# Performance work log

Hardware: AMD Instinct MI355X
Metric: run time of the kernel (lower is better)

## Reference

```python
import jax, jax.numpy as jnp
import numpy as np

N, IN_DIM, MLPW, HID, NCLS = 2048, 1024, 16, 256, 4


def setup_inputs() -> dict:
    key = jax.random.key(0)
    ks = jax.random.split(key, 12)
    f32 = jnp.float32
    return {
        "x": jax.random.normal(ks[0], (N, IN_DIM), f32),
        "adj": jax.random.uniform(ks[1], (N, N), f32),
        "xdeg": jax.random.uniform(ks[2], (N, N), f32),
        "ydeg": jax.random.uniform(ks[3], (N, N), f32),
        # edge MLP([3, mlp_width, 2])
        "Wm1": jax.random.normal(ks[4], (3, MLPW), f32) * (1.0 / np.sqrt(3.0)),
        "bm1": jnp.zeros((MLPW,), f32),
        "Wm2": jax.random.normal(ks[5], (MLPW, 2), f32) * (1.0 / np.sqrt(MLPW)),
        "bm2": jnp.zeros((2,), f32),
        # GCN / dense layers (stored as [in, out]; torch Linear applies x @ W.T)
        "Wg1": jax.random.normal(ks[6], (IN_DIM, HID), f32) * (1.0 / np.sqrt(IN_DIM)),
        "Wl2": jax.random.normal(ks[7], (HID, 64), f32) * (1.0 / np.sqrt(HID)),
        "bl2": jnp.zeros((64,), f32),
        "Wg2": jax.random.normal(ks[8], (64, NCLS), f32) * (1.0 / 8.0),
    }


def reference(x, adj, xdeg, ydeg, Wm1, bm1, Wm2, bm2, Wg1, Wl2, bl2, Wg2):
    n = adj.shape[0]
    # Edge-feature MLP mask. The torch code gathers nonzero entries, runs the
    # MLP, scatters back into a zero buffer, then multiplies by adj. Computing
    # the mask densely is mathematically identical because adj * mask is zero
    # wherever adj is zero.
    feats = jnp.stack([adj, xdeg, ydeg], axis=-1)          # [N, N, 3]
    h = jax.nn.relu(feats @ Wm1 + bm1)                     # [N, N, MLPW]
    mask = jax.nn.softmax(h @ Wm2 + bm2, axis=-1)[..., 1]  # [N, N]
    A = adj * mask + jnp.eye(n, dtype=adj.dtype)
    # Symmetric-ish normalization: D_row^{-1/2} A D_col^{-1/2}
    # (the torch diag-matmul chain reduces to this row/col scaling).
    rowsum = jnp.sum(A, axis=1)
    colsum = jnp.sum(A, axis=0)
    dr = jnp.where(rowsum > 0, jax.lax.rsqrt(jnp.where(rowsum > 0, rowsum, 1.0)), 0.0)
    dc = jnp.where(colsum > 0, jax.lax.rsqrt(jnp.where(colsum > 0, colsum, 1.0)), 0.0)
    A = dr[:, None] * A * dc[None, :]
    # GCN layer 1 (dropout = identity in eval mode)
    hid = (A @ (x @ Wg1)) @ Wl2 + bl2                      # [N, 64]
    # GCN layer 2
    out = A @ (hid @ Wg2)                                  # [N, n_classes]
    return out, hid
```

## Files before the change

kernel.cpp:

```cpp
#include <hip/hip_runtime.h>

#define NN 2048
#define MLPW 16

typedef __attribute__((ext_vector_type(8))) short short8v;
typedef __attribute__((ext_vector_type(16))) float float16v;
typedef __attribute__((ext_vector_type(4))) unsigned short ushort4v;
typedef __attribute__((ext_vector_type(8))) unsigned short ushort8v;

__device__ __forceinline__ unsigned short f2b(float f) {
  unsigned int u = __float_as_uint(f);
  unsigned int r = (u + 0x7fffu + ((u >> 16) & 1u)) >> 16;
  return (unsigned short)r;
}
__device__ __forceinline__ float b2f(unsigned short u) {
  return __uint_as_float(((unsigned int)u) << 16);
}

__global__ void __launch_bounds__(256) edge_kernel(
    const float* __restrict__ adj, const float* __restrict__ xdeg,
    const float* __restrict__ ydeg,
    const float* __restrict__ Wm1, const float* __restrict__ bm1,
    const float* __restrict__ Wm2, const float* __restrict__ bm2,
    unsigned short* __restrict__ Abf, float* __restrict__ dr) {
  __shared__ float w1[48], b1[16], w2[32], b2s[2];
  __shared__ float wsum[4];
  const int tid = threadIdx.x;
  if (tid < 48) w1[tid] = Wm1[tid];
  if (tid < 16) b1[tid] = bm1[tid];
  if (tid < 32) w2[tid] = Wm2[tid];
  if (tid < 2) b2s[tid] = bm2[tid];
  __syncthreads();
  const int i = blockIdx.x;
  const float4* adj4 = (const float4*)(adj + (size_t)i * NN);
  const float4* xd4 = (const float4*)(xdeg + (size_t)i * NN);
  const float4* yd4 = (const float4*)(ydeg + (size_t)i * NN);
  ushort4v* A4 = (ushort4v*)(Abf + (size_t)i * NN);
  float rsum = 0.f;
  for (int j4 = tid; j4 < NN / 4; j4 += 256) {
    float4 av = adj4[j4], xv = xd4[j4], yv = yd4[j4];
    float aa[4] = {av.x, av.y, av.z, av.w};
    float xx[4] = {xv.x, xv.y, xv.z, xv.w};
    float yy[4] = {yv.x, yv.y, yv.z, yv.w};
    ushort4v oo;
#pragma unroll
    for (int e = 0; e < 4; e++) {
      float l0 = b2s[0], l1 = b2s[1];
#pragma unroll
      for (int k = 0; k < MLPW; k++) {
        float h = fmaf(aa[e], w1[k], fmaf(xx[e], w1[16 + k], fmaf(yy[e], w1[32 + k], b1[k])));
        h = fmaxf(h, 0.f);
        l0 = fmaf(h, w2[2 * k], l0);
        l1 = fmaf(h, w2[2 * k + 1], l1);
      }
      float mask = 1.f / (1.f + __expf(l0 - l1));
      float v = aa[e] * mask;
      int j = j4 * 4 + e;
      if (j == i) v += 1.f;
      oo[e] = f2b(v);
      rsum += v;
    }
    A4[j4] = oo;
  }
#pragma unroll
  for (int off = 32; off > 0; off >>= 1) rsum += __shfl_down(rsum, off);
  if ((tid & 63) == 0) wsum[tid >> 6] = rsum;
  __syncthreads();
  if (tid == 0) {
    float t = wsum[0] + wsum[1] + wsum[2] + wsum[3];
    dr[i] = t > 0.f ? rsqrtf(t) : 0.f;
  }
}

__global__ void __launch_bounds__(256) aux_kernel(
    const unsigned short* __restrict__ Abf, const float* __restrict__ x,
    const float* __restrict__ Wg1, float* __restrict__ partial,
    unsigned short* __restrict__ xb, unsigned short* __restrict__ Wg1T) {
  const int b = blockIdx.x, tid = threadIdx.x;
  if (b < 256) {
    const int j0 = tid * 8, i0 = b * 8;
    float s[8] = {0, 0, 0, 0, 0, 0, 0, 0};
#pragma unroll
    for (int i = 0; i < 8; i++) {
      ushort8v a = *(const ushort8v*)&Abf[(size_t)(i0 + i) * NN + j0];
#pragma unroll
      for (int e = 0; e < 8; e++) s[e] += b2f(a[e]);
    }
    float* p = partial + (size_t)b * NN + j0;
    *(float4*)p = make_float4(s[0], s[1], s[2], s[3]);
    *(float4*)(p + 4) = make_float4(s[4], s[5], s[6], s[7]);
  } else if (b < 1280) {
    const size_t idx = (size_t)(b - 256) * 2048 + (size_t)tid * 8;
    const float4 u = *(const float4*)&x[idx], v = *(const float4*)&x[idx + 4];
    ushort8v o = {f2b(u.x), f2b(u.y), f2b(u.z), f2b(u.w),
                  f2b(v.x), f2b(v.y), f2b(v.z), f2b(v.w)};
    *(ushort8v*)&xb[idx] = o;
  } else {
    const int bo = b - 1280;
    const int n = bo * 2 + (tid >> 7);
    const int k0 = (tid & 127) * 8;
    ushort8v o;
#pragma unroll
    for (int e = 0; e < 8; e++) o[e] = f2b(Wg1[(size_t)(k0 + e) * 256 + n]);
    *(ushort8v*)&Wg1T[(size_t)n * 1024 + k0] = o;
  }
}

__global__ void __launch_bounds__(256) dc_kernel(
    const float* __restrict__ partial, float* __restrict__ dc) {
  __shared__ float red[8][32];
  const int l = threadIdx.x & 31, g = threadIdx.x >> 5;
  const int col = blockIdx.x * 32 + l;
  float s = 0.f;
#pragma unroll
  for (int q = 0; q < 32; q++) s += partial[(size_t)(g * 32 + q) * NN + col];
  red[g][l] = s;
  __syncthreads();
  if (g == 0) {
    float t = s;
#pragma unroll
    for (int gg = 1; gg < 8; gg++) t += red[gg][l];
    dc[col] = t > 0.f ? rsqrtf(t) : 0.f;
  }
}

__global__ void __launch_bounds__(256) gemm_splitk_kernel(
    const unsigned short* __restrict__ A, const unsigned short* __restrict__ B,
    float* __restrict__ P, int M, int N, int K, int Kc) {
  constexpr int SW = 136;
  __shared__ unsigned short As[64 * SW];
  __shared__ unsigned short Bs[128 * SW];
  const int tid = threadIdx.x;
  const int lane = tid & 63, wave = tid >> 6;
  const int l31 = lane & 31, half = lane >> 5;
  const int mh = wave & 1, nh = wave >> 1;
  const int row0 = blockIdx.y * 64, col0 = blockIdx.x * 128;
  const int kbeg = blockIdx.z * Kc;

  float16v acc0, acc1;
#pragma unroll
  for (int r = 0; r < 16; r++) { acc0[r] = 0.f; acc1[r] = 0.f; }

  for (int k0 = 0; k0 < Kc; k0 += 128) {
#pragma unroll
    for (int i = 0; i < 4; i++) {
      const int id = tid + i * 256;
      const int r = id >> 4, c = id & 15;
      *(ushort8v*)&As[r * SW + c * 8] =
          *(const ushort8v*)&A[(size_t)(row0 + r) * K + kbeg + k0 + c * 8];
    }
#pragma unroll
    for (int i = 0; i < 8; i++) {
      const int id = tid + i * 256;
      const int r = id >> 4, c = id & 15;
      *(ushort8v*)&Bs[r * SW + c * 8] =
          *(const ushort8v*)&B[(size_t)(col0 + r) * K + kbeg + k0 + c * 8];
    }
    __syncthreads();
#pragma unroll
    for (int ks = 0; ks < 8; ks++) {
      short8v a = *(const short8v*)&As[(mh * 32 + l31) * SW + ks * 16 + half * 8];
      short8v b0 = *(const short8v*)&Bs[(nh * 64 + l31) * SW + ks * 16 + half * 8];
      short8v b1 = *(const short8v*)&Bs[(nh * 64 + 32 + l31) * SW + ks * 16 + half * 8];
      acc0 = __builtin_amdgcn_mfma_f32_32x32x16_bf16(a, b0, acc0, 0, 0, 0);
      acc1 = __builtin_amdgcn_mfma_f32_32x32x16_bf16(a, b1, acc1, 0, 0, 0);
    }
    __syncthreads();
  }
  float* Pb = P + ((size_t)blockIdx.z * M + row0 + mh * 32) * N + col0 + nh * 64 + l31;
#pragma unroll
  for (int reg = 0; reg < 16; reg++) {
    const int m = (reg & 3) + 8 * (reg >> 2) + 4 * half;
    Pb[(size_t)m * N] = acc0[reg];
    Pb[(size_t)m * N + 32] = acc1[reg];
  }
}

__global__ void __launch_bounds__(256) reduce_xwt_kernel(
    const float* __restrict__ P, const float* __restrict__ dc,
    unsigned short* __restrict__ XWT) {
  const int t = blockIdx.x * 256 + threadIdx.x;
  const int i = t >> 8;
  const int j0 = (t & 255) * 8;
  float s[8] = {0, 0, 0, 0, 0, 0, 0, 0};
#pragma unroll
  for (int sk = 0; sk < 8; sk++) {
    const float* p = P + ((size_t)sk * 256 + i) * 2048 + j0;
    float4 u = *(const float4*)p, v = *(const float4*)(p + 4);
    s[0] += u.x; s[1] += u.y; s[2] += u.z; s[3] += u.w;
    s[4] += v.x; s[5] += v.y; s[6] += v.z; s[7] += v.w;
  }
  float4 d0 = *(const float4*)&dc[j0], d1 = *(const float4*)&dc[j0 + 4];
  ushort8v o = {f2b(s[0] * d0.x), f2b(s[1] * d0.y), f2b(s[2] * d0.z), f2b(s[3] * d0.w),
                f2b(s[4] * d1.x), f2b(s[5] * d1.y), f2b(s[6] * d1.z), f2b(s[7] * d1.w)};
  *(ushort8v*)&XWT[(size_t)i * 2048 + j0] = o;
}

__global__ void __launch_bounds__(256) tail_kernel(
    const float* __restrict__ P2, const float* __restrict__ dr,
    const float* __restrict__ dc, const float* __restrict__ Wl2,
    const float* __restrict__ bl2, const float* __restrict__ Wg2,
    float* __restrict__ hid, float* __restrict__ HW) {
  __shared__ float T1s[8][256];
  __shared__ float hidS[8][68];
  const int m0 = blockIdx.x * 8;
  const int tid = threadIdx.x;
#pragma unroll
  for (int i = 0; i < 8; i++) {
    const int idx = tid + i * 256;
    const int mi = idx >> 8, n = idx & 255;
    float s = 0.f;
#pragma unroll
    for (int sk = 0; sk < 8; sk++)
      s += P2[((size_t)sk * 2048 + m0 + mi) * 256 + n];
    T1s[mi][n] = s * dr[m0 + mi];
  }
  __syncthreads();
  const int j = tid & 63, mg = tid >> 6;
  float h0 = bl2[j], h1 = h0;
  for (int n = 0; n < 256; n++) {
    float w = Wl2[(size_t)n * 64 + j];
    h0 = fmaf(T1s[mg * 2 + 0][n], w, h0);
    h1 = fmaf(T1s[mg * 2 + 1][n], w, h1);
  }
  hid[(size_t)(m0 + mg * 2 + 0) * 64 + j] = h0;
  hid[(size_t)(m0 + mg * 2 + 1) * 64 + j] = h1;
  hidS[mg * 2 + 0][j] = h0;
  hidS[mg * 2 + 1][j] = h1;
  __syncthreads();
  if (tid < 32) {
    const int r = tid >> 2, c = tid & 3;
    float s = 0.f;
#pragma unroll
    for (int jj = 0; jj < 64; jj++) s = fmaf(hidS[r][jj], Wg2[jj * 4 + c], s);
    HW[(size_t)(m0 + r) * 4 + c] = s * dc[m0 + r];
  }
}

__global__ void __launch_bounds__(256) out_kernel(
    const unsigned short* __restrict__ Abf, const float* __restrict__ HW,
    const float* __restrict__ dr, float* __restrict__ outp) {
  const int i = blockIdx.x, tid = threadIdx.x;
  const ushort8v a8 = ((const ushort8v*)(Abf + (size_t)i * NN))[tid];
  const float4* hw4 = (const float4*)HW;
  const int j0 = tid * 8;
  float ax = 0.f, ay = 0.f, az = 0.f, aw = 0.f;
#pragma unroll
  for (int e = 0; e < 8; e++) {
    float a = b2f(a8[e]);
    float4 h = hw4[j0 + e];
    ax = fmaf(a, h.x, ax);
    ay = fmaf(a, h.y, ay);
    az = fmaf(a, h.z, az);
    aw = fmaf(a, h.w, aw);
  }
#pragma unroll
  for (int off = 32; off > 0; off >>= 1) {
    ax += __shfl_down(ax, off);
    ay += __shfl_down(ay, off);
    az += __shfl_down(az, off);
    aw += __shfl_down(aw, off);
  }
  __shared__ float wsum[4][4];
  const int w = tid >> 6;
  if ((tid & 63) == 0) {
    wsum[w][0] = ax; wsum[w][1] = ay; wsum[w][2] = az; wsum[w][3] = aw;
  }
  __syncthreads();
  if (tid < 4)
    outp[(size_t)i * 4 + tid] =
        dr[i] * (wsum[0][tid] + wsum[1][tid] + wsum[2][tid] + wsum[3][tid]);
}

extern "C" void kernel_launch(void* const* d_in, const int* in_sizes, int n_in,
                              void* d_out, int out_size, void* d_ws, size_t ws_size,
                              hipStream_t stream) {
  const float* x    = (const float*)d_in[0];
  const float* adj  = (const float*)d_in[1];
  const float* xdeg = (const float*)d_in[2];
  const float* ydeg = (const float*)d_in[3];
  const float* Wm1  = (const float*)d_in[4];
  const float* bm1  = (const float*)d_in[5];
  const float* Wm2  = (const float*)d_in[6];
  const float* bm2  = (const float*)d_in[7];
  const float* Wg1  = (const float*)d_in[8];
  const float* Wl2  = (const float*)d_in[9];
  const float* bl2  = (const float*)d_in[10];
  const float* Wg2  = (const float*)d_in[11];

  char* ws = (char*)d_ws;
  unsigned short* Abf  = (unsigned short*)(ws);
  unsigned short* XWT  = (unsigned short*)(ws + 8388608);
  float* P     = (float*)(ws + 9437184);
  float* part  = (float*)(ws + 26214400);
  unsigned short* xb   = (unsigned short*)(ws + 28311552);
  unsigned short* Wg1T = (unsigned short*)(ws + 32505856);
  float* dr    = (float*)(ws + 33030144);
  float* dc    = (float*)(ws + 33038336);
  float* HW    = (float*)(ws + 33046528);

  float* outp = (float*)d_out;
  float* hid  = (float*)d_out + 2048 * 4;

  edge_kernel<<<NN, 256, 0, stream>>>(adj, xdeg, ydeg, Wm1, bm1, Wm2, bm2, Abf, dr);
  aux_kernel<<<1408, 256, 0, stream>>>(Abf, x, Wg1, part, xb, Wg1T);
  dc_kernel<<<64, 256, 0, stream>>>(part, dc);
  gemm_splitk_kernel<<<dim3(2048 / 128, 256 / 64, 8), 256, 0, stream>>>(
      Wg1T, xb, P, 256, 2048, 1024, 128);
  reduce_xwt_kernel<<<256, 256, 0, stream>>>(P, dc, XWT);
  gemm_splitk_kernel<<<dim3(256 / 128, 2048 / 64, 8), 256, 0, stream>>>(
      Abf, XWT, P, 2048, 256, 2048, 256);
  tail_kernel<<<2048 / 8, 256, 0, stream>>>(P, dr, dc, Wl2, bl2, Wg2, hid, HW);
  out_kernel<<<NN, 256, 0, stream>>>(Abf, HW, dr, outp);
}
```

Before: 172.6 us.

## Fuse edge MLP with fp32-staged X·Wg1 GEMM and merge dc/reduce kernels

```diff
diff --git a/kernel.cpp b/kernel.cpp
--- a/kernel.cpp
+++ b/kernel.cpp
@@ -17,111 +17,173 @@
   return __uint_as_float(((unsigned int)u) << 16);
 }
 
-__global__ void __launch_bounds__(256) edge_kernel(
+__global__ void __launch_bounds__(256, 4) fused1_kernel(
     const float* __restrict__ adj, const float* __restrict__ xdeg,
     const float* __restrict__ ydeg,
     const float* __restrict__ Wm1, const float* __restrict__ bm1,
     const float* __restrict__ Wm2, const float* __restrict__ bm2,
-    unsigned short* __restrict__ Abf, float* __restrict__ dr) {
-  __shared__ float w1[48], b1[16], w2[32], b2s[2];
-  __shared__ float wsum[4];
+    const float* __restrict__ x, const float* __restrict__ Wg1,
+    unsigned short* __restrict__ Abf, float* __restrict__ dr,
+    float* __restrict__ P1) {
+  constexpr int SW = 136;
+  __shared__ unsigned short As[64 * SW];
+  __shared__ unsigned short Bs[64 * SW];
+  __shared__ float w1[48], b1[16], w2[32], b2s[2], wsum[4];
   const int tid = threadIdx.x;
-  if (tid < 48) w1[tid] = Wm1[tid];
-  if (tid < 16) b1[tid] = bm1[tid];
-  if (tid < 32) w2[tid] = Wm2[tid];
-  if (tid < 2) b2s[tid] = bm2[tid];
-  __syncthreads();
-  const int i = blockIdx.x;
-  const float4* adj4 = (const float4*)(adj + (size_t)i * NN);
-  const float4* xd4 = (const float4*)(xdeg + (size_t)i * NN);
-  const float4* yd4 = (const float4*)(ydeg + (size_t)i * NN);
-  ushort4v* A4 = (ushort4v*)(Abf + (size_t)i * NN);
-  float rsum = 0.f;
-  for (int j4 = tid; j4 < NN / 4; j4 += 256) {
-    float4 av = adj4[j4], xv = xd4[j4], yv = yd4[j4];
-    float aa[4] = {av.x, av.y, av.z, av.w};
-    float xx[4] = {xv.x, xv.y, xv.z, xv.w};
-    float yy[4] = {yv.x, yv.y, yv.z, yv.w};
-    ushort4v oo;
-#pragma unroll
-    for (int e = 0; e < 4; e++) {
-      float l0 = b2s[0], l1 = b2s[1];
-#pragma unroll
-      for (int k = 0; k < MLPW; k++) {
-        float h = fmaf(aa[e], w1[k], fmaf(xx[e], w1[16 + k], fmaf(yy[e], w1[32 + k], b1[k])));
-        h = fmaxf(h, 0.f);
-        l0 = fmaf(h, w2[2 * k], l0);
-        l1 = fmaf(h, w2[2 * k + 1], l1);
+
+  if (blockIdx.x < 512) {
+    const int bg = blockIdx.x;
+    const int sk = bg >> 7, rem = bg & 127;
+    const int row0 = (rem >> 5) * 64;
+    const int col0 = (rem & 31) * 64;
+    const int kbeg = sk * 256;
+    const int lane = tid & 63, wave = tid >> 6;
+    const int l31 = lane & 31, half = lane >> 5;
+    const int mh2 = (wave & 1) * 32, nh2 = (wave >> 1) * 32;
+    const int k2 = (tid & 63) * 2;
+    const int mh = (tid >> 6) * 16;
+    const int rB = tid >> 2, cB = (tid & 3) * 32;
+
+    float16v acc;
+#pragma unroll
+    for (int r = 0; r < 16; r++) acc[r] = 0.f;
+
+    for (int k0 = 0; k0 < 256; k0 += 128) {
+      const float* a0 = Wg1 + (size_t)(kbeg + k0 + k2) * 256 + row0 + mh;
+      const float* a1 = a0 + 256;
+#pragma unroll
+      for (int q = 0; q < 4; q++) {
+        float4 va = ((const float4*)a0)[q];
+        float4 vb = ((const float4*)a1)[q];
+        ushort2 u;
+        u.x = f2b(va.x); u.y = f2b(vb.x); *(ushort2*)&As[(mh + q * 4 + 0) * SW + k2] = u;
+        u.x = f2b(va.y); u.y = f2b(vb.y); *(ushort2*)&As[(mh + q * 4 + 1) * SW + k2] = u;
+        u.x = f2b(va.z); u.y = f2b(vb.z); *(ushort2*)&As[(mh + q * 4 + 2) * SW + k2] = u;
+        u.x = f2b(va.w); u.y = f2b(vb.w); *(ushort2*)&As[(mh + q * 4 + 3) * SW + k2] = u;
       }
-      float mask = 1.f / (1.f + __expf(l0 - l1));
-      float v = aa[e] * mask;
-      int j = j4 * 4 + e;
-      if (j == i) v += 1.f;
-      oo[e] = f2b(v);
-      rsum += v;
-    }
-    A4[j4] = oo;
-  }
-#pragma unroll
-  for (int off = 32; off > 0; off >>= 1) rsum += __shfl_down(rsum, off);
-  if ((tid & 63) == 0) wsum[tid >> 6] = rsum;
-  __syncthreads();
-  if (tid == 0) {
-    float t = wsum[0] + wsum[1] + wsum[2] + wsum[3];
-    dr[i] = t > 0.f ? rsqrtf(t) : 0.f;
-  }
-}
-
-__global__ void __launch_bounds__(256) aux_kernel(
-    const unsigned short* __restrict__ Abf, const float* __restrict__ x,
-    const float* __restrict__ Wg1, float* __restrict__ partial,
-    unsigned short* __restrict__ xb, unsigned short* __restrict__ Wg1T) {
-  const int b = blockIdx.x, tid = threadIdx.x;
-  if (b < 256) {
-    const int j0 = tid * 8, i0 = b * 8;
-    float s[8] = {0, 0, 0, 0, 0, 0, 0, 0};
-#pragma unroll
-    for (int i = 0; i < 8; i++) {
-      ushort8v a = *(const ushort8v*)&Abf[(size_t)(i0 + i) * NN + j0];
-#pragma unroll
-      for (int e = 0; e < 8; e++) s[e] += b2f(a[e]);
-    }
-    float* p = partial + (size_t)b * NN + j0;
-    *(float4*)p = make_float4(s[0], s[1], s[2], s[3]);
-    *(float4*)(p + 4) = make_float4(s[4], s[5], s[6], s[7]);
-  } else if (b < 1280) {
-    const size_t idx = (size_t)(b - 256) * 2048 + (size_t)tid * 8;
-    const float4 u = *(const float4*)&x[idx], v = *(const float4*)&x[idx + 4];
-    ushort8v o = {f2b(u.x), f2b(u.y), f2b(u.z), f2b(u.w),
-                  f2b(v.x), f2b(v.y), f2b(v.z), f2b(v.w)};
-    *(ushort8v*)&xb[idx] = o;
+      const float* bp = x + (size_t)(col0 + rB) * 1024 + kbeg + k0 + cB;
+#pragma unroll
+      for (int q = 0; q < 4; q++) {
+        float4 u = ((const float4*)bp)[2 * q], v = ((const float4*)bp)[2 * q + 1];
+        ushort8v pk = {f2b(u.x), f2b(u.y), f2b(u.z), f2b(u.w),
+                       f2b(v.x), f2b(v.y), f2b(v.z), f2b(v.w)};
+        *(ushort8v*)&Bs[rB * SW + cB + q * 8] = pk;
+      }
+      __syncthreads();
+#pragma unroll
+      for (int ks = 0; ks < 8; ks++) {
+        short8v a = *(const short8v*)&As[(mh2 + l31) * SW + ks * 16 + half * 8];
+        short8v b = *(const short8v*)&Bs[(nh2 + l31) * SW + ks * 16 + half * 8];
+        acc = __builtin_amdgcn_mfma_f32_32x32x16_bf16(a, b, acc, 0, 0, 0);
+      }
+      __syncthreads();
+    }
+    float* Pb = P1 + ((size_t)sk * 256 + row0 + mh2) * NN + col0 + nh2 + l31;
+#pragma unroll
+    for (int reg = 0; reg < 16; reg++) {
+      const int m = (reg & 3) + 8 * (reg >> 2) + 4 * half;
+      Pb[(size_t)m * NN] = acc[reg];
+    }
   } else {
-    const int bo = b - 1280;
-    const int n = bo * 2 + (tid >> 7);
-    const int k0 = (tid & 127) * 8;
-    ushort8v o;
-#pragma unroll
-    for (int e = 0; e < 8; e++) o[e] = f2b(Wg1[(size_t)(k0 + e) * 256 + n]);
-    *(ushort8v*)&Wg1T[(size_t)n * 1024 + k0] = o;
-  }
-}
-
-__global__ void __launch_bounds__(256) dc_kernel(
-    const float* __restrict__ partial, float* __restrict__ dc) {
-  __shared__ float red[8][32];
-  const int l = threadIdx.x & 31, g = threadIdx.x >> 5;
-  const int col = blockIdx.x * 32 + l;
-  float s = 0.f;
-#pragma unroll
-  for (int q = 0; q < 32; q++) s += partial[(size_t)(g * 32 + q) * NN + col];
-  red[g][l] = s;
-  __syncthreads();
-  if (g == 0) {
-    float t = s;
-#pragma unroll
-    for (int gg = 1; gg < 8; gg++) t += red[gg][l];
-    dc[col] = t > 0.f ? rsqrtf(t) : 0.f;
-  }
+    if (tid < 48) w1[tid] = Wm1[tid];
+    if (tid < 16) b1[tid] = bm1[tid];
+    if (tid < 32) w2[tid] = Wm2[tid];
+    if (tid < 2) b2s[tid] = bm2[tid];
+    __syncthreads();
+    const int i = blockIdx.x - 512;
+    const float4* adj4 = (const float4*)(adj + (size_t)i * NN);
+    const float4* xd4 = (const float4*)(xdeg + (size_t)i * NN);
+    const float4* yd4 = (const float4*)(ydeg + (size_t)i * NN);
+    ushort4v* A4 = (ushort4v*)(Abf + (size_t)i * NN);
+    float rsum = 0.f;
+    for (int j4 = tid; j4 < NN / 4; j4 += 256) {
+      float4 av = adj4[j4], xv = xd4[j4], yv = yd4[j4];
+      float aa[4] = {av.x, av.y, av.z, av.w};
+      float xx[4] = {xv.x, xv.y, xv.z, xv.w};
+      float yy[4] = {yv.x, yv.y, yv.z, yv.w};
+      ushort4v oo;
+#pragma unroll
+      for (int e = 0; e < 4; e++) {
+        float l0 = b2s[0], l1 = b2s[1];
+#pragma unroll
+        for (int k = 0; k < MLPW; k++) {
+          float h = fmaf(aa[e], w1[k], fmaf(xx[e], w1[16 + k], fmaf(yy[e], w1[32 + k], b1[k])));
+          h = fmaxf(h, 0.f);
+          l0 = fmaf(h, w2[2 * k], l0);
+          l1 = fmaf(h, w2[2 * k + 1], l1);
+        }
+        float mask = 1.f / (1.f + __expf(l0 - l1));
+        float v = aa[e] * mask;
+        int j = j4 * 4 + e;
+        if (j == i) v += 1.f;
+        oo[e] = f2b(v);
+        rsum += v;
+      }
+      A4[j4] = oo;
+    }
+#pragma unroll
+    for (int off = 32; off > 0; off >>= 1) rsum += __shfl_down(rsum, off);
+    if ((tid & 63) == 0) wsum[tid >> 6] = rsum;
+    __syncthreads();
+    if (tid == 0) {
+      float t = wsum[0] + wsum[1] + wsum[2] + wsum[3];
+      dr[i] = t > 0.f ? rsqrtf(t) : 0.f;
+    }
+  }
+}
+
+__global__ void __launch_bounds__(256) dcxwt_kernel(
+    const unsigned short* __restrict__ Abf, const float* __restrict__ P1,
+    float* __restrict__ dc, unsigned short* __restrict__ XWT) {
+  __shared__ float partA[32][16];
+  __shared__ float dcs[16];
+  const int tid = threadIdx.x;
+  const int c0 = blockIdx.x * 16;
+  {
+    const int c2 = (tid & 7) * 2, rg = tid >> 3;
+    float s0 = 0.f, s1 = 0.f;
+    const unsigned short* ap = Abf + (size_t)rg * NN + c0 + c2;
+#pragma unroll 8
+    for (int k = 0; k < 64; k++) {
+      ushort2 u = *(const ushort2*)ap;
+      s0 += b2f(u.x);
+      s1 += b2f(u.y);
+      ap += 32 * NN;
+    }
+    partA[rg][c2] = s0;
+    partA[rg][c2 + 1] = s1;
+  }
+  __syncthreads();
+  if (tid < 16) {
+    float d = 0.f;
+#pragma unroll
+    for (int rg = 0; rg < 32; rg++) d += partA[rg][tid];
+    d = d > 0.f ? rsqrtf(d) : 0.f;
+    dcs[tid] = d;
+    dc[c0 + tid] = d;
+  }
+  __syncthreads();
+  float s[16];
+#pragma unroll
+  for (int e = 0; e < 16; e++) s[e] = 0.f;
+#pragma unroll
+  for (int sk = 0; sk < 4; sk++) {
+    const float* p = P1 + ((size_t)sk * 256 + tid) * NN + c0;
+    float4 u0 = ((const float4*)p)[0], u1 = ((const float4*)p)[1];
+    float4 u2 = ((const float4*)p)[2], u3 = ((const float4*)p)[3];
+    s[0] += u0.x; s[1] += u0.y; s[2] += u0.z; s[3] += u0.w;
+    s[4] += u1.x; s[5] += u1.y; s[6] += u1.z; s[7] += u1.w;
+    s[8] += u2.x; s[9] += u2.y; s[10] += u2.z; s[11] += u2.w;
+    s[12] += u3.x; s[13] += u3.y; s[14] += u3.z; s[15] += u3.w;
+  }
+  ushort8v o0 = {f2b(s[0] * dcs[0]), f2b(s[1] * dcs[1]), f2b(s[2] * dcs[2]),
+                 f2b(s[3] * dcs[3]), f2b(s[4] * dcs[4]), f2b(s[5] * dcs[5]),
+                 f2b(s[6] * dcs[6]), f2b(s[7] * dcs[7])};
+  ushort8v o1 = {f2b(s[8] * dcs[8]), f2b(s[9] * dcs[9]), f2b(s[10] * dcs[10]),
+                 f2b(s[11] * dcs[11]), f2b(s[12] * dcs[12]), f2b(s[13] * dcs[13]),
+                 f2b(s[14] * dcs[14]), f2b(s[15] * dcs[15])};
+  *(ushort8v*)&XWT[(size_t)tid * NN + c0] = o0;
+  *(ushort8v*)&XWT[(size_t)tid * NN + c0 + 8] = o1;
 }
 
 __global__ void __launch_bounds__(256) gemm_splitk_kernel(
@@ -176,35 +238,21 @@
   }
 }
 
-__global__ void __launch_bounds__(256) reduce_xwt_kernel(
-    const float* __restrict__ P, const float* __restrict__ dc,
-    unsigned short* __restrict__ XWT) {
-  const int t = blockIdx.x * 256 + threadIdx.x;
-  const int i = t >> 8;
-  const int j0 = (t & 255) * 8;
-  float s[8] = {0, 0, 0, 0, 0, 0, 0, 0};
-#pragma unroll
-  for (int sk = 0; sk < 8; sk++) {
-    const float* p = P + ((size_t)sk * 256 + i) * 2048 + j0;
-    float4 u = *(const float4*)p, v = *(const float4*)(p + 4);
-    s[0] += u.x; s[1] += u.y; s[2] += u.z; s[3] += u.w;
-    s[4] += v.x; s[5] += v.y; s[6] += v.z; s[7] += v.w;
-  }
-  float4 d0 = *(const float4*)&dc[j0], d1 = *(const float4*)&dc[j0 + 4];
-  ushort8v o = {f2b(s[0] * d0.x), f2b(s[1] * d0.y), f2b(s[2] * d0.z), f2b(s[3] * d0.w),
-                f2b(s[4] * d1.x), f2b(s[5] * d1.y), f2b(s[6] * d1.z), f2b(s[7] * d1.w)};
-  *(ushort8v*)&XWT[(size_t)i * 2048 + j0] = o;
-}
-
 __global__ void __launch_bounds__(256) tail_kernel(
     const float* __restrict__ P2, const float* __restrict__ dr,
     const float* __restrict__ dc, const float* __restrict__ Wl2,
     const float* __restrict__ bl2, const float* __restrict__ Wg2,
     float* __restrict__ hid, float* __restrict__ HW) {
   __shared__ float T1s[8][256];
+  __shared__ float Wl2s[256 * 64];
   __shared__ float hidS[8][68];
   const int m0 = blockIdx.x * 8;
   const int tid = threadIdx.x;
+#pragma unroll
+  for (int k = 0; k < 16; k++) {
+    const int idx = (tid + k * 256) * 4;
+    *(float4*)&Wl2s[idx] = *(const float4*)&Wl2[idx];
+  }
 #pragma unroll
   for (int i = 0; i < 8; i++) {
     const int idx = tid + i * 256;
@@ -218,8 +266,9 @@
   __syncthreads();
   const int j = tid & 63, mg = tid >> 6;
   float h0 = bl2[j], h1 = h0;
+#pragma unroll 8
   for (int n = 0; n < 256; n++) {
-    float w = Wl2[(size_t)n * 64 + j];
+    float w = Wl2s[n * 64 + j];
     h0 = fmaf(T1s[mg * 2 + 0][n], w, h0);
     h1 = fmaf(T1s[mg * 2 + 1][n], w, h1);
   }
@@ -289,27 +338,22 @@
   const float* Wg2  = (const float*)d_in[11];
 
   char* ws = (char*)d_ws;
-  unsigned short* Abf  = (unsigned short*)(ws);
-  unsigned short* XWT  = (unsigned short*)(ws + 8388608);
-  float* P     = (float*)(ws + 9437184);
-  float* part  = (float*)(ws + 26214400);
-  unsigned short* xb   = (unsigned short*)(ws + 28311552);
-  unsigned short* Wg1T = (unsigned short*)(ws + 32505856);
-  float* dr    = (float*)(ws + 33030144);
-  float* dc    = (float*)(ws + 33038336);
-  float* HW    = (float*)(ws + 33046528);
+  unsigned short* Abf = (unsigned short*)(ws);
+  float* P1   = (float*)(ws + 8388608);
+  unsigned short* XWT = (unsigned short*)(ws + 16777216);
+  float* P2   = (float*)(ws + 17825792);
+  float* dr   = (float*)(ws + 34603008);
+  float* dc   = (float*)(ws + 34611200);
+  float* HW   = (float*)(ws + 34619392);
 
   float* outp = (float*)d_out;
   float* hid  = (float*)d_out + 2048 * 4;
 
-  edge_kernel<<<NN, 256, 0, stream>>>(adj, xdeg, ydeg, Wm1, bm1, Wm2, bm2, Abf, dr);
-  aux_kernel<<<1408, 256, 0, stream>>>(Abf, x, Wg1, part, xb, Wg1T);
-  dc_kernel<<<64, 256, 0, stream>>>(part, dc);
-  gemm_splitk_kernel<<<dim3(2048 / 128, 256 / 64, 8), 256, 0, stream>>>(
-      Wg1T, xb, P, 256, 2048, 1024, 128);
-  reduce_xwt_kernel<<<256, 256, 0, stream>>>(P, dc, XWT);
+  fused1_kernel<<<2560, 256, 0, stream>>>(adj, xdeg, ydeg, Wm1, bm1, Wm2, bm2,
+                                          x, Wg1, Abf, dr, P1);
+  dcxwt_kernel<<<128, 256, 0, stream>>>(Abf, P1, dc, XWT);
   gemm_splitk_kernel<<<dim3(256 / 128, 2048 / 64, 8), 256, 0, stream>>>(
-      Abf, XWT, P, 2048, 256, 2048, 256);
-  tail_kernel<<<2048 / 8, 256, 0, stream>>>(P, dr, dc, Wl2, bl2, Wg2, hid, HW);
+      Abf, XWT, P2, 2048, 256, 2048, 256);
+  tail_kernel<<<2048 / 8, 256, 0, stream>>>(P2, dr, dc, Wl2, bl2, Wg2, hid, HW);
   out_kernel<<<NN, 256, 0, stream>>>(Abf, HW, dr, outp);
 }
```

Result: slower. 311.6 us (+80.6%).

## Fuse conversions into edge kernel and merge column-sum with split-K reduce

Applied to the files above, without the earlier changes.

```diff
diff --git a/kernel.cpp b/kernel.cpp
--- a/kernel.cpp
+++ b/kernel.cpp
@@ -22,16 +22,37 @@
     const float* __restrict__ ydeg,
     const float* __restrict__ Wm1, const float* __restrict__ bm1,
     const float* __restrict__ Wm2, const float* __restrict__ bm2,
-    unsigned short* __restrict__ Abf, float* __restrict__ dr) {
+    const float* __restrict__ x, const float* __restrict__ Wg1,
+    unsigned short* __restrict__ Abf, float* __restrict__ dr,
+    unsigned short* __restrict__ xb, unsigned short* __restrict__ Wg1T) {
+  const int tid = threadIdx.x;
+  const int b = blockIdx.x;
+  if (b >= 3072) {
+    const int bo = b - 3072;
+    const int n = bo * 2 + (tid >> 7);
+    const int k0 = (tid & 127) * 8;
+    ushort8v o;
+#pragma unroll
+    for (int e = 0; e < 8; e++) o[e] = f2b(Wg1[(size_t)(k0 + e) * 256 + n]);
+    *(ushort8v*)&Wg1T[(size_t)n * 1024 + k0] = o;
+    return;
+  }
+  if (b >= 2048) {
+    const size_t idx = (size_t)(b - 2048) * 2048 + (size_t)tid * 8;
+    const float4 u = *(const float4*)&x[idx], v = *(const float4*)&x[idx + 4];
+    ushort8v o = {f2b(u.x), f2b(u.y), f2b(u.z), f2b(u.w),
+                  f2b(v.x), f2b(v.y), f2b(v.z), f2b(v.w)};
+    *(ushort8v*)&xb[idx] = o;
+    return;
+  }
   __shared__ float w1[48], b1[16], w2[32], b2s[2];
   __shared__ float wsum[4];
-  const int tid = threadIdx.x;
   if (tid < 48) w1[tid] = Wm1[tid];
   if (tid < 16) b1[tid] = bm1[tid];
   if (tid < 32) w2[tid] = Wm2[tid];
   if (tid < 2) b2s[tid] = bm2[tid];
   __syncthreads();
-  const int i = blockIdx.x;
+  const int i = b;
   const float4* adj4 = (const float4*)(adj + (size_t)i * NN);
   const float4* xd4 = (const float4*)(xdeg + (size_t)i * NN);
   const float4* yd4 = (const float4*)(ydeg + (size_t)i * NN);
@@ -72,58 +93,6 @@
   }
 }
 
-__global__ void __launch_bounds__(256) aux_kernel(
-    const unsigned short* __restrict__ Abf, const float* __restrict__ x,
-    const float* __restrict__ Wg1, float* __restrict__ partial,
-    unsigned short* __restrict__ xb, unsigned short* __restrict__ Wg1T) {
-  const int b = blockIdx.x, tid = threadIdx.x;
-  if (b < 256) {
-    const int j0 = tid * 8, i0 = b * 8;
-    float s[8] = {0, 0, 0, 0, 0, 0, 0, 0};
-#pragma unroll
-    for (int i = 0; i < 8; i++) {
-      ushort8v a = *(const ushort8v*)&Abf[(size_t)(i0 + i) * NN + j0];
-#pragma unroll
-      for (int e = 0; e < 8; e++) s[e] += b2f(a[e]);
-    }
-    float* p = partial + (size_t)b * NN + j0;
-    *(float4*)p = make_float4(s[0], s[1], s[2], s[3]);
-    *(float4*)(p + 4) = make_float4(s[4], s[5], s[6], s[7]);
-  } else if (b < 1280) {
-    const size_t idx = (size_t)(b - 256) * 2048 + (size_t)tid * 8;
-    const float4 u = *(const float4*)&x[idx], v = *(const float4*)&x[idx + 4];
-    ushort8v o = {f2b(u.x), f2b(u.y), f2b(u.z), f2b(u.w),
-                  f2b(v.x), f2b(v.y), f2b(v.z), f2b(v.w)};
-    *(ushort8v*)&xb[idx] = o;
-  } else {
-    const int bo = b - 1280;
-    const int n = bo * 2 + (tid >> 7);
-    const int k0 = (tid & 127) * 8;
-    ushort8v o;
-#pragma unroll
-    for (int e = 0; e < 8; e++) o[e] = f2b(Wg1[(size_t)(k0 + e) * 256 + n]);
-    *(ushort8v*)&Wg1T[(size_t)n * 1024 + k0] = o;
-  }
-}
-
-__global__ void __launch_bounds__(256) dc_kernel(
-    const float* __restrict__ partial, float* __restrict__ dc) {
-  __shared__ float red[8][32];
-  const int l = threadIdx.x & 31, g = threadIdx.x >> 5;
-  const int col = blockIdx.x * 32 + l;
-  float s = 0.f;
-#pragma unroll
-  for (int q = 0; q < 32; q++) s += partial[(size_t)(g * 32 + q) * NN + col];
-  red[g][l] = s;
-  __syncthreads();
-  if (g == 0) {
-    float t = s;
-#pragma unroll
-    for (int gg = 1; gg < 8; gg++) t += red[gg][l];
-    dc[col] = t > 0.f ? rsqrtf(t) : 0.f;
-  }
-}
-
 __global__ void __launch_bounds__(256) gemm_splitk_kernel(
     const unsigned short* __restrict__ A, const unsigned short* __restrict__ B,
     float* __restrict__ P, int M, int N, int K, int Kc) {
@@ -176,24 +145,59 @@
   }
 }
 
-__global__ void __launch_bounds__(256) reduce_xwt_kernel(
-    const float* __restrict__ P, const float* __restrict__ dc,
-    unsigned short* __restrict__ XWT) {
-  const int t = blockIdx.x * 256 + threadIdx.x;
-  const int i = t >> 8;
-  const int j0 = (t & 255) * 8;
-  float s[8] = {0, 0, 0, 0, 0, 0, 0, 0};
+__global__ void __launch_bounds__(256) dcxwt_kernel(
+    const unsigned short* __restrict__ Abf, const float* __restrict__ P1,
+    float* __restrict__ dc, unsigned short* __restrict__ XWT) {
+  __shared__ float part[64][32];
+  __shared__ float dcs[32];
+  const int tid = threadIdx.x;
+  const int c0 = blockIdx.x * 32;
+  {
+    const int cA = (tid & 3) * 8, rgA = tid >> 2;
+    float sa[8] = {0, 0, 0, 0, 0, 0, 0, 0};
+    const unsigned short* ap = Abf + (size_t)rgA * NN + c0 + cA;
+#pragma unroll 4
+    for (int k = 0; k < 32; k++) {
+      ushort8v u = *(const ushort8v*)ap;
+#pragma unroll
+      for (int e = 0; e < 8; e++) sa[e] += b2f(u[e]);
+      ap += (size_t)64 * NN;
+    }
+#pragma unroll
+    for (int e = 0; e < 8; e++) part[rgA][cA + e] = sa[e];
+  }
+  __syncthreads();
+  if (tid < 32) {
+    float d = 0.f;
+#pragma unroll
+    for (int rg = 0; rg < 64; rg++) d += part[rg][tid];
+    d = d > 0.f ? rsqrtf(d) : 0.f;
+    dcs[tid] = d;
+    dc[c0 + tid] = d;
+  }
+  __syncthreads();
+  const int rB = tid >> 3, cq = (tid & 7) * 4;
+  float acc[8][4];
+#pragma unroll
+  for (int p = 0; p < 8; p++)
+#pragma unroll
+    for (int e = 0; e < 4; e++) acc[p][e] = 0.f;
 #pragma unroll
   for (int sk = 0; sk < 8; sk++) {
-    const float* p = P + ((size_t)sk * 256 + i) * 2048 + j0;
-    float4 u = *(const float4*)p, v = *(const float4*)(p + 4);
-    s[0] += u.x; s[1] += u.y; s[2] += u.z; s[3] += u.w;
-    s[4] += v.x; s[5] += v.y; s[6] += v.z; s[7] += v.w;
-  }
-  float4 d0 = *(const float4*)&dc[j0], d1 = *(const float4*)&dc[j0 + 4];
-  ushort8v o = {f2b(s[0] * d0.x), f2b(s[1] * d0.y), f2b(s[2] * d0.z), f2b(s[3] * d0.w),
-                f2b(s[4] * d1.x), f2b(s[5] * d1.y), f2b(s[6] * d1.z), f2b(s[7] * d1.w)};
-  *(ushort8v*)&XWT[(size_t)i * 2048 + j0] = o;
+#pragma unroll
+    for (int p = 0; p < 8; p++) {
+      const float* pp = P1 + ((size_t)sk * 256 + rB + p * 32) * NN + c0 + cq;
+      float4 v = *(const float4*)pp;
+      acc[p][0] += v.x; acc[p][1] += v.y; acc[p][2] += v.z; acc[p][3] += v.w;
+    }
+  }
+  const float4 dv = *(const float4*)&dcs[cq];
+#pragma unroll
+  for (int p = 0; p < 8; p++) {
+    ushort4v o = {f2b(acc[p][0] * dv.x), f2b(acc[p][1] * dv.y),
+                  f2b(acc[p][2] * dv.z), f2b(acc[p][3] * dv.w)};
+    *(ushort4v*)&XWT[(size_t)(rB + p * 32) * NN + c0 + cq] = o;
+  }
 }
 
 __global__ void __launch_bounds__(256) tail_kernel(
@@ -218,6 +222,7 @@
   __syncthreads();
   const int j = tid & 63, mg = tid >> 6;
   float h0 = bl2[j], h1 = h0;
+#pragma unroll 8
   for (int n = 0; n < 256; n++) {
     float w = Wl2[(size_t)n * 64 + j];
     h0 = fmaf(T1s[mg * 2 + 0][n], w, h0);
@@ -290,26 +295,25 @@
 
   char* ws = (char*)d_ws;
   unsigned short* Abf  = (unsigned short*)(ws);
-  unsigned short* XWT  = (unsigned short*)(ws + 8388608);
-  float* P     = (float*)(ws + 9437184);
-  float* part  = (float*)(ws + 26214400);
-  unsigned short* xb   = (unsigned short*)(ws + 28311552);
-  unsigned short* Wg1T = (unsigned short*)(ws + 32505856);
-  float* dr    = (float*)(ws + 33030144);
-  float* dc    = (float*)(ws + 33038336);
-  float* HW    = (float*)(ws + 33046528);
+  unsigned short* xb   = (unsigned short*)(ws + 8388608);
+  unsigned short* Wg1T = (unsigned short*)(ws + 12582912);
+  float* P1   = (float*)(ws + 13107200);
+  float* P2   = (float*)(ws + 29884416);
+  unsigned short* XWT = (unsigned short*)(ws + 46661632);
+  float* dr   = (float*)(ws + 47710208);
+  float* dc   = (float*)(ws + 47718400);
+  float* HW   = (float*)(ws + 47726592);
 
   float* outp = (float*)d_out;
   float* hid  = (float*)d_out + 2048 * 4;
 
-  edge_kernel<<<NN, 256, 0, stream>>>(adj, xdeg, ydeg, Wm1, bm1, Wm2, bm2, Abf, dr);
-  aux_kernel<<<1408, 256, 0, stream>>>(Abf, x, Wg1, part, xb, Wg1T);
-  dc_kernel<<<64, 256, 0, stream>>>(part, dc);
+  edge_kernel<<<3200, 256, 0, stream>>>(adj, xdeg, ydeg, Wm1, bm1, Wm2, bm2,
+                                        x, Wg1, Abf, dr, xb, Wg1T);
   gemm_splitk_kernel<<<dim3(2048 / 128, 256 / 64, 8), 256, 0, stream>>>(
-      Wg1T, xb, P, 256, 2048, 1024, 128);
-  reduce_xwt_kernel<<<256, 256, 0, stream>>>(P, dc, XWT);
+      Wg1T, xb, P1, 256, 2048, 1024, 128);
+  dcxwt_kernel<<<64, 256, 0, stream>>>(Abf, P1, dc, XWT);
   gemm_splitk_kernel<<<dim3(256 / 128, 2048 / 64, 8), 256, 0, stream>>>(
-      Abf, XWT, P, 2048, 256, 2048, 256);
-  tail_kernel<<<2048 / 8, 256, 0, stream>>>(P, dr, dc, Wl2, bl2, Wg2, hid, HW);
+      Abf, XWT, P2, 2048, 256, 2048, 256);
+  tail_kernel<<<2048 / 8, 256, 0, stream>>>(P2, dr, dc, Wl2, bl2, Wg2, hid, HW);
   out_kernel<<<NN, 256, 0, stream>>>(Abf, HW, dr, outp);
 }
```

After: 169.3 us. No clear change (-1.9%).
